# Kernel tuning notes

Measured on AMD Instinct MI355X. Metric: run time of the kernel, lower is better.

Reference implementation:

```python
import jax, jax.numpy as jnp
import numpy as np

H, C = 5, 64            # attention heads, per-head channels (out_channels=conv_dim)
NEG_SLOPE = 0.2         # GATv2 leaky_relu slope
N_NODES = 50000

def setup_inputs() -> dict:
    key = jax.random.key(0)
    ks = jax.random.split(key, 10)
    N, E = N_NODES, 400000
    node_dim, edge_dim = 128, 16
    s = 0.1
    return {
        'x': jax.random.normal(ks[0], (N, node_dim), jnp.float32),
        'edge_index': jax.random.randint(ks[1], (2, E), 0, N),
        'edge_attr': jax.random.normal(ks[2], (E, edge_dim), jnp.float32),
        'W0': jax.random.normal(ks[3], (node_dim, H * C), jnp.float32) * s,
        'b0': jnp.zeros((H * C,), jnp.float32),
        'We0': jax.random.normal(ks[4], (edge_dim, H * C), jnp.float32) * s,
        'att0': jax.random.normal(ks[5], (H, C), jnp.float32) * s,
        'bias0': jnp.zeros((C,), jnp.float32),
        'W12': jax.random.normal(ks[6], (2, C, H * C), jnp.float32) * s,
        'b12': jnp.zeros((2, H * C), jnp.float32),
        'We12': jax.random.normal(ks[7], (2, edge_dim, H * C), jnp.float32) * s,
        'att12': jax.random.normal(ks[8], (2, H, C), jnp.float32) * s,
        'bias12': jnp.zeros((2, C), jnp.float32),
    }

def _add_self_loops_mean(edge_index, edge_attr, N):
    # PyG add_self_loops(fill_value='mean'): self-loop attr = mean of incoming edge attrs per dst node
    dst = edge_index[1]
    sums = jax.ops.segment_sum(edge_attr, dst, num_segments=N)
    cnt = jax.ops.segment_sum(jnp.ones((edge_attr.shape[0], 1), edge_attr.dtype), dst, num_segments=N)
    loop_attr = sums / jnp.maximum(cnt, 1.0)
    loop = jnp.arange(N, dtype=edge_index.dtype)
    ei = jnp.concatenate([edge_index, jnp.stack([loop, loop])], axis=1)
    ea = jnp.concatenate([edge_attr, loop_attr], axis=0)
    return ei, ea

def _gatv2_layer(x, src, dst, eattr, W, b, We, att, bias, N):
    h = (x @ W + b).reshape(N, H, C)                     # shared lin_l==lin_r (share_weights=True)
    e = (eattr @ We).reshape(-1, H, C)                   # lin_edge (no bias)
    s = jax.nn.leaky_relu(h[src] + h[dst] + e, NEG_SLOPE)  # [E', H, C]
    logits = jnp.einsum('ehc,hc->eh', s, att)            # [E', H]
    m = jax.ops.segment_max(logits, dst, num_segments=N)
    m = jnp.where(jnp.isfinite(m), m, 0.0)
    ex = jnp.exp(logits - m[dst])
    denom = jax.ops.segment_sum(ex, dst, num_segments=N) + 1e-16
    alpha = ex / denom[dst]                              # per-dst softmax (dropout off: eval mode)
    msg = h[src] * alpha[:, :, None]
    out = jax.ops.segment_sum(msg, dst, num_segments=N)  # [N, H, C]
    return out.mean(axis=1) + bias                       # concat=False -> head mean, then bias

def reference(x, edge_index, edge_attr, W0, b0, We0, att0, bias0, W12, b12, We12, att12, bias12):
    N = x.shape[0]
    ei, ea = _add_self_loops_mean(edge_index, edge_attr, N)
    src, dst = ei[0], ei[1]
    h = jax.nn.elu(_gatv2_layer(x, src, dst, ea, W0, b0, We0, att0, bias0, N))
    for i in range(2):
        h = jax.nn.elu(_gatv2_layer(h, src, dst, ea, W12[i], b12[i], We12[i], att12[i], bias12[i], N))
    return h  # jk_mode='last'
```

## Files before the change

kernel.cpp:

```cpp
#include <hip/hip_runtime.h>
#include <hip/hip_fp16.h>
#include <math.h>

#define NH 5
#define NC 64
#define ED 16
#define HC 320
#define CH 32

typedef _Float16 h2  __attribute__((ext_vector_type(2)));
typedef _Float16 v4h __attribute__((ext_vector_type(4)));
typedef _Float16 v8h __attribute__((ext_vector_type(8)));
typedef float    v4f __attribute__((ext_vector_type(4)));

__device__ __forceinline__ float wave_sum_all(float x) {
    asm("v_add_f32_dpp %0, %1, %0 quad_perm:[1,0,3,2] row_mask:0xf bank_mask:0xf"
        : "+v"(x) : "v"(x));
    asm("v_add_f32_dpp %0, %1, %0 quad_perm:[2,3,0,1] row_mask:0xf bank_mask:0xf"
        : "+v"(x) : "v"(x));
    asm("v_add_f32_dpp %0, %1, %0 row_half_mirror row_mask:0xf bank_mask:0xf"
        : "+v"(x) : "v"(x));
    asm("v_add_f32_dpp %0, %1, %0 row_mirror row_mask:0xf bank_mask:0xf"
        : "+v"(x) : "v"(x));
    asm("v_add_f32_dpp %0, %1, %0 row_bcast:15 row_mask:0xa bank_mask:0xf"
        : "+v"(x) : "v"(x));
    asm("v_add_f32_dpp %0, %1, %0 row_bcast:31 row_mask:0xc bank_mask:0xf"
        : "+v"(x) : "v"(x));
    return __int_as_float(__builtin_amdgcn_readlane(__float_as_int(x), 63));
}


__global__ void count_kernel(const int* __restrict__ dst, int* __restrict__ cnt, int E) {
    int t = blockIdx.x * blockDim.x + threadIdx.x;
    if (t >= E) return;
    atomicAdd(&cnt[dst[t]], 1);
}

__global__ void scan_kernel(const int* __restrict__ cnt, int* __restrict__ offsets,
                            int* __restrict__ cursor, int N) {
    __shared__ int sums[1024];
    int t = threadIdx.x;
    int chunk = (N + 1023) / 1024;
    int beg = t * chunk;
    int end = min(beg + chunk, N);
    int s = 0;
    for (int i = beg; i < end; ++i) s += cnt[i] + 1;
    sums[t] = s;
    __syncthreads();
    for (int o = 1; o < 1024; o <<= 1) {
        int v = (t >= o) ? sums[t - o] : 0;
        __syncthreads();
        sums[t] += v;
        __syncthreads();
    }
    int run = (t > 0) ? sums[t - 1] : 0;
    for (int i = beg; i < end; ++i) {
        offsets[i] = run; cursor[i] = run;
        run += cnt[i] + 1;
    }
    if (t == 0) offsets[N] = sums[1023];
}

__global__ void scatter_kernel(const int* __restrict__ src, const int* __restrict__ dst,
                               int* __restrict__ cursor, int2* __restrict__ recs, int N, int E) {
    int t = blockIdx.x * blockDim.x + threadIdx.x;
    if (t >= E + N) return;
    int d, s;
    if (t < E) { d = dst[t]; s = src[t]; }
    else       { d = t - E; s = t - E; }
    int pos = atomicAdd(&cursor[d], 1);
    recs[pos] = make_int2(s, t);
}

__global__ void loop_from_csr(const int* __restrict__ offsets, const int2* __restrict__ recs,
                              const float* __restrict__ ea, float* __restrict__ loop,
                              int N, int E) {
    int t = blockIdx.x * blockDim.x + threadIdx.x;
    int n = t >> 4, k = t & 15;
    if (n >= N) return;
    int beg = offsets[n], end = offsets[n + 1];
    float s = 0.f; int c = 0;
    for (int j = beg; j < end; ++j) {
        int y = recs[j].y;
        if (y < E) { s += ea[(size_t)y * ED + k]; ++c; }
    }
    loop[(size_t)n * ED + k] = s / (float)max(c, 1);
}

__global__ void reorder_ea(const int2* __restrict__ recs, const float* __restrict__ ea,
                           const float* __restrict__ loop, h2* __restrict__ easrt,
                           int* __restrict__ srcs, int R, int E) {
    int t = blockIdx.x * blockDim.x + threadIdx.x;
    int slot = t >> 3, k2 = t & 7;
    if (slot >= R) return;
    int2 rc = recs[slot];
    if (k2 == 0) srcs[slot] = rc.x;
    int y = rc.y;
    const float2* sp = (const float2*)((y < E) ? ea + (size_t)y * ED : loop + (size_t)(y - E) * ED);
    float2 f = sp[k2];
    h2 o; o.x = (_Float16)f.x; o.y = (_Float16)f.y;
    easrt[(size_t)slot * 8 + k2] = o;
}

__global__ void win_start_kernel(const int* __restrict__ offsets, int* __restrict__ winStart, int N) {
    int i = blockIdx.x * blockDim.x + threadIdx.x;
    if (i >= N) return;
    atomicMin(&winStart[offsets[i] / CH], i);
}

__global__ void cvt_f16(const float* __restrict__ in, _Float16* __restrict__ out, int n) {
    int i = blockIdx.x * blockDim.x + threadIdx.x;
    if (i < n) out[i] = (_Float16)in[i];
}

__global__ void transpose_w(const float* __restrict__ W, _Float16* __restrict__ Wt, int K) {
    int t = blockIdx.x * blockDim.x + threadIdx.x;
    if (t >= 320 * K) return;
    int k = t / 320, n = t % 320;
    Wt[(size_t)n * K + k] = (_Float16)W[t];
}

__global__ __launch_bounds__(256) void gemm_mfma(const _Float16* __restrict__ A,
                                                 const _Float16* __restrict__ Bt,
                                                 const float* __restrict__ bias,
                                                 _Float16* __restrict__ CoutA,
                                                 _Float16* __restrict__ CoutB, int M, int K) {
    int lane = threadIdx.x & 63;
    int wave = threadIdx.x >> 6;
    int m = lane & 15, quad = lane >> 4;
    int rowBase = (blockIdx.x * 4 + wave) * 16;
    if (rowBase >= M) return;

    v4f acc[20];
#pragma unroll
    for (int c = 0; c < 20; ++c) acc[c] = (v4f){0.f, 0.f, 0.f, 0.f};

    for (int k0 = 0; k0 < K; k0 += 32) {
        v8h a = *(const v8h*)&A[(size_t)(rowBase + m) * K + k0 + quad * 8];
#pragma unroll
        for (int c = 0; c < 20; ++c) {
            v8h b = *(const v8h*)&Bt[(size_t)(c * 16 + m) * K + k0 + quad * 8];
            acc[c] = __builtin_amdgcn_mfma_f32_16x16x32_f16(a, b, acc[c], 0, 0, 0);
        }
    }
    float bb[20];
#pragma unroll
    for (int c = 0; c < 20; ++c) bb[c] = bias[c * 16 + m];
#pragma unroll
    for (int r = 0; r < 4; ++r) {
        int row = rowBase + quad * 4 + r;
#pragma unroll
        for (int c03 = 0; c03 < 4; ++c03) {
            v4h o;
#pragma unroll
            for (int h = 0; h < 4; ++h) {
                int c = c03 + 4 * h;
                o[h] = (_Float16)(acc[c][r] + bb[c]);
            }
            int cw = c03 * 16 + m;
            *(v4h*)&CoutA[(((size_t)row) * 64 + cw) * 4] = o;
            int c4 = c03 + 16;
            CoutB[((size_t)row) * 64 + cw] = (_Float16)(acc[c4][r] + bb[c4]);
        }
    }
}

__global__ __launch_bounds__(256) void gat_fused(const _Float16* __restrict__ hA,
                                                 const _Float16* __restrict__ hB,
                                                 const int* __restrict__ offsets,
                                                 const int* __restrict__ srcs,
                                                 const h2* __restrict__ easrt,
                                                 const int* __restrict__ winStart,
                                                 const float* __restrict__ We,
                                                 const float* __restrict__ att,
                                                 const float* __restrict__ bias,
                                                 _Float16* __restrict__ outH,
                                                 float* __restrict__ outF,
                                                 int N, int R) {
    int lane = threadIdx.x & 63;
    int wave = (blockIdx.x * blockDim.x + threadIdx.x) >> 6;
    int totalWaves = (gridDim.x * blockDim.x) >> 6;
    const float L2E = 1.4426950408889634f;

    h2 we2[8 * NH];
#pragma unroll
    for (int k2 = 0; k2 < 8; ++k2)
#pragma unroll
        for (int h = 0; h < NH; ++h) {
            h2 w;
            w.x = (_Float16)We[(2 * k2) * HC + h * NC + lane];
            w.y = (_Float16)We[(2 * k2 + 1) * HC + h * NC + lane];
            we2[k2 * NH + h] = w;
        }
    float attc6[NH], attc4[NH];
#pragma unroll
    for (int h = 0; h < NH; ++h) {
        float a = att[h * NC + lane];
        attc6[h] = 0.6f * L2E * a;
        attc4[h] = 0.4f * L2E * a;
    }
    float bc = bias[lane];

    for (int w = wave; w * CH < R; w += totalWaves) {
        int i = winStart[w];
        if (i >= N) continue;
        int winEnd = w * CH + CH;
        for (; i < N; ++i) {
            int beg = offsets[i];
            if (beg >= winEnd) break;
            int end = offsets[i + 1];

            v4h hd4 = *(const v4h*)&hA[((size_t)i * 64 + lane) * 4];
            float hd[NH];
#pragma unroll
            for (int h = 0; h < 4; ++h) hd[h] = (float)hd4[h];
            hd[4] = (float)hB[(size_t)i * 64 + lane];

            float l[NH] = {}, acc[NH] = {};
            int t = beg;
            for (; t + 2 <= end; t += 2) {
                int s0 = srcs[t], s1 = srcs[t + 1];
                v4h hs0v = *(const v4h*)&hA[((size_t)s0 * 64 + lane) * 4];
                v4h hs1v = *(const v4h*)&hA[((size_t)s1 * 64 + lane) * 4];
                _Float16 hs0e = hB[(size_t)s0 * 64 + lane];
                _Float16 hs1e = hB[(size_t)s1 * 64 + lane];
                const h2* ap = easrt + (size_t)t * 8;
                h2 a0[8], a1[8];
#pragma unroll
                for (int k2 = 0; k2 < 8; ++k2) { a0[k2] = ap[k2]; a1[k2] = ap[8 + k2]; }
                float hs0[NH], hs1[NH], p0[NH], p1[NH];
#pragma unroll
                for (int h = 0; h < 4; ++h) { hs0[h] = (float)hs0v[h]; hs1[h] = (float)hs1v[h]; }
                hs0[4] = (float)hs0e; hs1[4] = (float)hs1e;
#pragma unroll
                for (int h = 0; h < NH; ++h) {
                    float v0 = hs0[h] + hd[h];
                    float v1 = hs1[h] + hd[h];
#pragma unroll
                    for (int k2 = 0; k2 < 8; ++k2) {
                        v0 = __builtin_amdgcn_fdot2(a0[k2], we2[k2 * NH + h], v0, false);
                        v1 = __builtin_amdgcn_fdot2(a1[k2], we2[k2 * NH + h], v1, false);
                    }
                    p0[h] = fmaf(fabsf(v0), attc4[h], v0 * attc6[h]);
                    p1[h] = fmaf(fabsf(v1), attc4[h], v1 * attc6[h]);
                }
#pragma unroll
                for (int h = 0; h < NH; ++h) {
                    float pe0 = exp2f(wave_sum_all(p0[h]));
                    float pe1 = exp2f(wave_sum_all(p1[h]));
                    l[h] += pe0 + pe1;
                    acc[h] = fmaf(pe0, hs0[h], fmaf(pe1, hs1[h], acc[h]));
                }
            }
            if (t < end) {
                int s0 = srcs[t];
                v4h hs0v = *(const v4h*)&hA[((size_t)s0 * 64 + lane) * 4];
                _Float16 hs0e = hB[(size_t)s0 * 64 + lane];
                const h2* ap = easrt + (size_t)t * 8;
                h2 a0[8];
#pragma unroll
                for (int k2 = 0; k2 < 8; ++k2) a0[k2] = ap[k2];
                float hs0[NH];
#pragma unroll
                for (int h = 0; h < 4; ++h) hs0[h] = (float)hs0v[h];
                hs0[4] = (float)hs0e;
#pragma unroll
                for (int h = 0; h < NH; ++h) {
                    float v0 = hs0[h] + hd[h];
#pragma unroll
                    for (int k2 = 0; k2 < 8; ++k2)
                        v0 = __builtin_amdgcn_fdot2(a0[k2], we2[k2 * NH + h], v0, false);
                    float pe0 = exp2f(wave_sum_all(fmaf(fabsf(v0), attc4[h], v0 * attc6[h])));
                    l[h] += pe0;
                    acc[h] = fmaf(pe0, hs0[h], acc[h]);
                }
            }
            float o = 0.f;
#pragma unroll
            for (int h = 0; h < NH; ++h) o += acc[h] / l[h];
            o = o * 0.2f + bc;
            o = o > 0.f ? o : expm1f(o);
            if (outF) outF[(size_t)i * NC + lane] = o;
            else      outH[(size_t)i * NC + lane] = (_Float16)o;
        }
    }
}

extern "C" void kernel_launch(void* const* d_in, const int* in_sizes, int n_in,
                              void* d_out, int out_size, void* d_ws, size_t ws_size,
                              hipStream_t stream) {
    const float* x     = (const float*)d_in[0];
    const int*   ei    = (const int*)d_in[1];
    const float* ea    = (const float*)d_in[2];
    const float* W0    = (const float*)d_in[3];
    const float* b0    = (const float*)d_in[4];
    const float* We0   = (const float*)d_in[5];
    const float* att0  = (const float*)d_in[6];
    const float* bias0 = (const float*)d_in[7];
    const float* W12   = (const float*)d_in[8];
    const float* b12   = (const float*)d_in[9];
    const float* We12  = (const float*)d_in[10];
    const float* att12 = (const float*)d_in[11];
    const float* bias12= (const float*)d_in[12];

    int N = in_sizes[0] / 128;
    int E = in_sizes[1] / 2;
    int R = E + N;
    int numWin = (R + CH - 1) / CH;
    const int* srcArr = ei;
    const int* dstArr = ei + E;

    char* ws = (char*)d_ws;
    size_t off = 0;
    auto alloc = [&](size_t bytes) -> void* {
        void* p = ws + off;
        off = (off + bytes + 255) & ~(size_t)255;
        return p;
    };
    int*      cnt     = (int*)alloc((size_t)N * 4);
    int*      offsets = (int*)alloc((size_t)(N + 1) * 4);
    int*      cursor  = (int*)alloc((size_t)N * 4);
    int2*     recs    = (int2*)alloc((size_t)R * 8);
    float*    loop    = (float*)alloc((size_t)N * ED * 4);
    _Float16* hbufA   = (_Float16*)alloc((size_t)N * 64 * 4 * 2);
    _Float16* hbufB   = (_Float16*)alloc((size_t)N * 64 * 2);
    _Float16* acth    = (_Float16*)alloc((size_t)N * NC * 2);
    _Float16* xh      = (_Float16*)alloc((size_t)N * 128 * 2);
    _Float16* Wth0    = (_Float16*)alloc((size_t)320 * 128 * 2);
    _Float16* Wth1    = (_Float16*)alloc((size_t)320 * 64 * 2);
    _Float16* Wth2    = (_Float16*)alloc((size_t)320 * 64 * 2);
    int*      winStart= (int*)alloc((size_t)(numWin + 1) * 4);
    h2*       easrt   = (h2*)alloc((size_t)R * 32);
    int*      srcs    = (int*)alloc((size_t)R * 4);

    (void)hipMemsetAsync(cnt, 0, (size_t)N * 4, stream);
    (void)hipMemsetAsync(winStart, 0x7f, (size_t)(numWin + 1) * 4, stream);
    count_kernel<<<(E + 255) / 256, 256, 0, stream>>>(dstArr, cnt, E);
    scan_kernel<<<1, 1024, 0, stream>>>(cnt, offsets, cursor, N);
    scatter_kernel<<<(E + N + 255) / 256, 256, 0, stream>>>(srcArr, dstArr, cursor, recs, N, E);
    loop_from_csr<<<((size_t)N * ED + 255) / 256, 256, 0, stream>>>(offsets, recs, ea, loop, N, E);
    reorder_ea<<<((size_t)R * 8 + 255) / 256, 256, 0, stream>>>(recs, ea, loop, easrt, srcs, R, E);
    win_start_kernel<<<(N + 255) / 256, 256, 0, stream>>>(offsets, winStart, N);
    cvt_f16<<<((size_t)N * 128 + 255) / 256, 256, 0, stream>>>(x, xh, N * 128);
    transpose_w<<<(320 * 128 + 255) / 256, 256, 0, stream>>>(W0, Wth0, 128);
    transpose_w<<<(320 * 64 + 255) / 256, 256, 0, stream>>>(W12, Wth1, 64);
    transpose_w<<<(320 * 64 + 255) / 256, 256, 0, stream>>>(W12 + 64 * HC, Wth2, 64);

    float* dout = (float*)d_out;
    int gemmBlocks = (N / 16 + 3) / 4 + 1;
    int fusedBlocks = (numWin + 3) / 4;

    const _Float16* As[3]  = {xh, acth, acth};
    const _Float16* Bts[3] = {Wth0, Wth1, Wth2};
    int Ks[3] = {128, 64, 64};
    const float* bs[3]   = {b0, b12, b12 + HC};
    const float* Wes[3]  = {We0, We12, We12 + ED * HC};
    const float* atts[3] = {att0, att12, att12 + NH * NC};
    const float* bis[3]  = {bias0, bias12, bias12 + NC};
    for (int layer = 0; layer < 3; ++layer) {
        gemm_mfma<<<gemmBlocks, 256, 0, stream>>>(As[layer], Bts[layer], bs[layer],
                                                  hbufA, hbufB, N, Ks[layer]);
        gat_fused<<<fusedBlocks, 256, 0, stream>>>(hbufA, hbufB, offsets, srcs, easrt, winStart,
                                                   Wes[layer], atts[layer], bis[layer],
                                                   acth, (layer == 2) ? dout : nullptr, N, R);
    }
}
```

Baseline: 851.2 us.

## Fuse x conversion into GEMM, compute self-loop attrs from sorted fp16 edges, add setprio

The first-layer GEMM now reads fp32 x directly and converts to fp16 in registers, which removes the separate cvt_f16 kernel and its fp16 copy of x. The self-loop mean edge attribute is no longer computed by a separate fp32 pass over CSR records. Instead, scatter records each node's self-loop slot and a new loop_fill kernel averages the already reordered fp16 edge attributes in place. The mean is therefore taken over fp16-rounded values, with a small precision change. s_setprio hints are also added around the compute section of the fused attention loop.

```diff
diff --git a/kernel.cpp b/kernel.cpp
--- a/kernel.cpp
+++ b/kernel.cpp
@@ -62,7 +62,8 @@
 }
 
 __global__ void scatter_kernel(const int* __restrict__ src, const int* __restrict__ dst,
-                               int* __restrict__ cursor, int2* __restrict__ recs, int N, int E) {
+                               int* __restrict__ cursor, int2* __restrict__ recs,
+                               int* __restrict__ selfSlot, int N, int E) {
     int t = blockIdx.x * blockDim.x + threadIdx.x;
     if (t >= E + N) return;
     int d, s;
@@ -70,36 +71,40 @@
     else       { d = t - E; s = t - E; }
     int pos = atomicAdd(&cursor[d], 1);
     recs[pos] = make_int2(s, t);
-}
-
-__global__ void loop_from_csr(const int* __restrict__ offsets, const int2* __restrict__ recs,
-                              const float* __restrict__ ea, float* __restrict__ loop,
-                              int N, int E) {
-    int t = blockIdx.x * blockDim.x + threadIdx.x;
-    int n = t >> 4, k = t & 15;
-    if (n >= N) return;
-    int beg = offsets[n], end = offsets[n + 1];
-    float s = 0.f; int c = 0;
-    for (int j = beg; j < end; ++j) {
-        int y = recs[j].y;
-        if (y < E) { s += ea[(size_t)y * ED + k]; ++c; }
-    }
-    loop[(size_t)n * ED + k] = s / (float)max(c, 1);
+    if (t >= E) selfSlot[d] = pos;
 }
 
 __global__ void reorder_ea(const int2* __restrict__ recs, const float* __restrict__ ea,
-                           const float* __restrict__ loop, h2* __restrict__ easrt,
-                           int* __restrict__ srcs, int R, int E) {
+                           h2* __restrict__ easrt, int* __restrict__ srcs, int R, int E) {
     int t = blockIdx.x * blockDim.x + threadIdx.x;
     int slot = t >> 3, k2 = t & 7;
     if (slot >= R) return;
     int2 rc = recs[slot];
     if (k2 == 0) srcs[slot] = rc.x;
     int y = rc.y;
-    const float2* sp = (const float2*)((y < E) ? ea + (size_t)y * ED : loop + (size_t)(y - E) * ED);
+    if (y >= E) return;
+    const float2* sp = (const float2*)(ea + (size_t)y * ED);
     float2 f = sp[k2];
     h2 o; o.x = (_Float16)f.x; o.y = (_Float16)f.y;
     easrt[(size_t)slot * 8 + k2] = o;
+}
+
+__global__ void loop_fill(const int* __restrict__ offsets, const int* __restrict__ selfSlot,
+                          h2* __restrict__ easrt, int N) {
+    int t = blockIdx.x * blockDim.x + threadIdx.x;
+    int n = t >> 3, k2 = t & 7;
+    if (n >= N) return;
+    int beg = offsets[n], end = offsets[n + 1];
+    int ss = selfSlot[n];
+    float sx = 0.f, sy = 0.f;
+    for (int j = beg; j < end; ++j) {
+        if (j == ss) continue;
+        h2 v = easrt[(size_t)j * 8 + k2];
+        sx += (float)v.x; sy += (float)v.y;
+    }
+    float inv = 1.f / (float)max(end - beg - 1, 1);
+    h2 o; o.x = (_Float16)(sx * inv); o.y = (_Float16)(sy * inv);
+    easrt[(size_t)ss * 8 + k2] = o;
 }
 
 __global__ void win_start_kernel(const int* __restrict__ offsets, int* __restrict__ winStart, int N) {
@@ -108,11 +113,6 @@
     atomicMin(&winStart[offsets[i] / CH], i);
 }
 
-__global__ void cvt_f16(const float* __restrict__ in, _Float16* __restrict__ out, int n) {
-    int i = blockIdx.x * blockDim.x + threadIdx.x;
-    if (i < n) out[i] = (_Float16)in[i];
-}
-
 __global__ void transpose_w(const float* __restrict__ W, _Float16* __restrict__ Wt, int K) {
     int t = blockIdx.x * blockDim.x + threadIdx.x;
     if (t >= 320 * K) return;
@@ -120,7 +120,8 @@
     Wt[(size_t)n * K + k] = (_Float16)W[t];
 }
 
-__global__ __launch_bounds__(256) void gemm_mfma(const _Float16* __restrict__ A,
+__global__ __launch_bounds__(256) void gemm_mfma(const _Float16* __restrict__ Ah,
+                                                 const float* __restrict__ Af,
                                                  const _Float16* __restrict__ Bt,
                                                  const float* __restrict__ bias,
                                                  _Float16* __restrict__ CoutA,
@@ -136,7 +137,18 @@
     for (int c = 0; c < 20; ++c) acc[c] = (v4f){0.f, 0.f, 0.f, 0.f};
 
     for (int k0 = 0; k0 < K; k0 += 32) {
-        v8h a = *(const v8h*)&A[(size_t)(rowBase + m) * K + k0 + quad * 8];
+        v8h a;
+        if (Af) {
+            const float* ap = &Af[(size_t)(rowBase + m) * K + k0 + quad * 8];
+            float4 f0 = *(const float4*)ap;
+            float4 f1 = *(const float4*)(ap + 4);
+            a[0] = (_Float16)f0.x; a[1] = (_Float16)f0.y;
+            a[2] = (_Float16)f0.z; a[3] = (_Float16)f0.w;
+            a[4] = (_Float16)f1.x; a[5] = (_Float16)f1.y;
+            a[6] = (_Float16)f1.z; a[7] = (_Float16)f1.w;
+        } else {
+            a = *(const v8h*)&Ah[(size_t)(rowBase + m) * K + k0 + quad * 8];
+        }
 #pragma unroll
         for (int c = 0; c < 20; ++c) {
             v8h b = *(const v8h*)&Bt[(size_t)(c * 16 + m) * K + k0 + quad * 8];
@@ -228,6 +240,7 @@
                 h2 a0[8], a1[8];
 #pragma unroll
                 for (int k2 = 0; k2 < 8; ++k2) { a0[k2] = ap[k2]; a1[k2] = ap[8 + k2]; }
+                __builtin_amdgcn_s_setprio(1);
                 float hs0[NH], hs1[NH], p0[NH], p1[NH];
 #pragma unroll
                 for (int h = 0; h < 4; ++h) { hs0[h] = (float)hs0v[h]; hs1[h] = (float)hs1v[h]; }
@@ -251,6 +264,7 @@
                     l[h] += pe0 + pe1;
                     acc[h] = fmaf(pe0, hs0[h], fmaf(pe1, hs1[h], acc[h]));
                 }
+                __builtin_amdgcn_s_setprio(0);
             }
             if (t < end) {
                 int s0 = srcs[t];
@@ -321,11 +335,10 @@
     int*      offsets = (int*)alloc((size_t)(N + 1) * 4);
     int*      cursor  = (int*)alloc((size_t)N * 4);
     int2*     recs    = (int2*)alloc((size_t)R * 8);
-    float*    loop    = (float*)alloc((size_t)N * ED * 4);
+    int*      selfSlot= (int*)alloc((size_t)N * 4);
     _Float16* hbufA   = (_Float16*)alloc((size_t)N * 64 * 4 * 2);
     _Float16* hbufB   = (_Float16*)alloc((size_t)N * 64 * 2);
     _Float16* acth    = (_Float16*)alloc((size_t)N * NC * 2);
-    _Float16* xh      = (_Float16*)alloc((size_t)N * 128 * 2);
     _Float16* Wth0    = (_Float16*)alloc((size_t)320 * 128 * 2);
     _Float16* Wth1    = (_Float16*)alloc((size_t)320 * 64 * 2);
     _Float16* Wth2    = (_Float16*)alloc((size_t)320 * 64 * 2);
@@ -337,11 +350,11 @@
     (void)hipMemsetAsync(winStart, 0x7f, (size_t)(numWin + 1) * 4, stream);
     count_kernel<<<(E + 255) / 256, 256, 0, stream>>>(dstArr, cnt, E);
     scan_kernel<<<1, 1024, 0, stream>>>(cnt, offsets, cursor, N);
-    scatter_kernel<<<(E + N + 255) / 256, 256, 0, stream>>>(srcArr, dstArr, cursor, recs, N, E);
-    loop_from_csr<<<((size_t)N * ED + 255) / 256, 256, 0, stream>>>(offsets, recs, ea, loop, N, E);
-    reorder_ea<<<((size_t)R * 8 + 255) / 256, 256, 0, stream>>>(recs, ea, loop, easrt, srcs, R, E);
+    scatter_kernel<<<(E + N + 255) / 256, 256, 0, stream>>>(srcArr, dstArr, cursor, recs,
+                                                            selfSlot, N, E);
+    reorder_ea<<<((size_t)R * 8 + 255) / 256, 256, 0, stream>>>(recs, ea, easrt, srcs, R, E);
+    loop_fill<<<((size_t)N * 8 + 255) / 256, 256, 0, stream>>>(offsets, selfSlot, easrt, N);
     win_start_kernel<<<(N + 255) / 256, 256, 0, stream>>>(offsets, winStart, N);
-    cvt_f16<<<((size_t)N * 128 + 255) / 256, 256, 0, stream>>>(x, xh, N * 128);
     transpose_w<<<(320 * 128 + 255) / 256, 256, 0, stream>>>(W0, Wth0, 128);
     transpose_w<<<(320 * 64 + 255) / 256, 256, 0, stream>>>(W12, Wth1, 64);
     transpose_w<<<(320 * 64 + 255) / 256, 256, 0, stream>>>(W12 + 64 * HC, Wth2, 64);
@@ -350,7 +363,8 @@
     int gemmBlocks = (N / 16 + 3) / 4 + 1;
     int fusedBlocks = (numWin + 3) / 4;
 
-    const _Float16* As[3]  = {xh, acth, acth};
+    const _Float16* Ahs[3] = {nullptr, acth, acth};
+    const float*    Afs[3] = {x, nullptr, nullptr};
     const _Float16* Bts[3] = {Wth0, Wth1, Wth2};
     int Ks[3] = {128, 64, 64};
     const float* bs[3]   = {b0, b12, b12 + HC};
@@ -358,7 +372,7 @@
     const float* atts[3] = {att0, att12, att12 + NH * NC};
     const float* bis[3]  = {bias0, bias12, bias12 + NC};
     for (int layer = 0; layer < 3; ++layer) {
-        gemm_mfma<<<gemmBlocks, 256, 0, stream>>>(As[layer], Bts[layer], bs[layer],
+        gemm_mfma<<<gemmBlocks, 256, 0, stream>>>(Ahs[layer], Afs[layer], Bts[layer], bs[layer],
                                                   hbufA, hbufB, N, Ks[layer]);
         gat_fused<<<fusedBlocks, 256, 0, stream>>>(hbufA, hbufB, offsets, srcs, easrt, winStart,
                                                    Wes[layer], atts[layer], bis[layer],
```

Result: faster. 821.7 us (-3.5%).
